# Optimization experiments

Measured on AMD Instinct MI355X. Metric: run time of the kernel, lower is better.

Reference implementation:

```python
import jax, jax.numpy as jnp
import numpy as np

N = 16384      # tokens (batch*seq)
D = 2048       # input_size / d_model
E = 64         # num_experts
K = 2          # top_k
EPS = 1e-12    # F.normalize eps


def setup_inputs() -> dict:
    key = jax.random.key(0)
    k1, k2 = jax.random.split(key)
    x = jax.random.normal(k1, (N, D), dtype=jnp.float32)
    # nn.Linear(input_size, num_experts, bias=False) weight has shape [E, D]
    W = jax.random.normal(k2, (E, D), dtype=jnp.float32) / np.sqrt(D)
    return {"x": x, "W": W}


def reference(x, W):
    # router logits: [N, E], computed (and kept) in float32 as in .float()
    logits = jnp.matmul(x, W.T).astype(jnp.float32)

    top_k_logits, top_k_indices = jax.lax.top_k(logits, K)      # [N, K]
    top_k_gates = jax.nn.softmax(top_k_logits, axis=1).astype(x.dtype)

    # ---- training-mode aux loss ----
    probs = jax.nn.softmax(logits, axis=1)                      # [N, E]
    rows = jnp.arange(logits.shape[0])[:, None]                 # [N, 1]
    gates = jnp.zeros_like(probs).astype(top_k_gates.dtype)
    gates = gates.at[rows, top_k_indices].set(top_k_gates)      # dense [N, E]

    count = logits.shape[0]
    p_sum = probs.sum(axis=0)                                   # [E]
    freq = (gates > 0).astype(jnp.float32).sum(axis=0)          # [E]
    lse = jax.nn.logsumexp(logits, axis=-1)                     # [N]
    lsesq = jnp.sum(lse ** 2)

    p_norm = p_sum / jnp.maximum(jnp.sum(jnp.abs(p_sum)), EPS)   # L1 normalize
    f_norm = freq / jnp.maximum(jnp.sum(jnp.abs(freq)), EPS)
    switchloss = E * jnp.sum(p_norm * f_norm)
    z_loss = lsesq / count
    loss = switchloss + 0.1 * z_loss

    return top_k_indices, top_k_gates, loss
```

## Files before the change

### kernel.cpp

```cpp
#include <hip/hip_runtime.h>
#include <hip/hip_bf16.h>
#include <math.h>

#define N_TOK 16384
#define D_DIM 2048
#define E_EXP 64
#define KQ    256
#define NKS   16
#define NBLK  256

typedef __attribute__((ext_vector_type(8))) short bf16x8;
typedef __attribute__((ext_vector_type(16))) float f32x16;
typedef __attribute__((ext_vector_type(4))) unsigned int u32x4;

#define PACK2(HI, LO) __builtin_amdgcn_perm((HI), (LO), 0x07060302u)

typedef union { unsigned u[4]; bf16x8 v; } b8u;

__global__ void pack_w(const float* __restrict__ W,
                       unsigned short* __restrict__ Wp) {
  const int T = blockIdx.x * 256 + threadIdx.x;
  const int e = T & 63, j = (T >> 6) & 3, c = T >> 8;
  const float* src = W + (size_t)e * D_DIM + c * 32 + j * 8;
  float4 v0 = *(const float4*)src;
  float4 v1 = *(const float4*)(src + 4);
  float vv[8] = {v0.x, v0.y, v0.z, v0.w, v1.x, v1.y, v1.z, v1.w};
  unsigned hu[8], mu[8], lu[8];
#pragma unroll
  for (int q = 0; q < 8; ++q) {
    unsigned u = __float_as_uint(vv[q]);
    unsigned a = u & 0xffff0000u;
    float r = vv[q] - __uint_as_float(a);
    unsigned b = __float_as_uint(r) & 0xffff0000u;
    float r2 = r - __uint_as_float(b);
    unsigned d = __float_as_uint(r2) & 0xffff0000u;
    hu[q] = a; mu[q] = b; lu[q] = d;
  }
  u32x4 ph, pm, pl;
#pragma unroll
  for (int q = 0; q < 4; ++q) {
    ph[q] = PACK2(hu[2 * q + 1], hu[2 * q]);
    pm[q] = PACK2(mu[2 * q + 1], mu[2 * q]);
    pl[q] = PACK2(lu[2 * q + 1], lu[2 * q]);
  }
  const size_t base = (size_t)c * 6144 + (j >> 1) * 3072 + (j & 1) * 512 + e * 8;
  *(u32x4*)(Wp + base)        = ph;
  *(u32x4*)(Wp + base + 1024) = pm;
  *(u32x4*)(Wp + base + 2048) = pl;
}

struct KSst {
  float4 a0, a1, c0, c1;
  bf16x8 B0h, B0m, B0l, B1h, B1m, B1l;
};

__global__ __launch_bounds__(512)
void fused_router(const float* __restrict__ x,
                  const unsigned short* __restrict__ Wp,
                  float* __restrict__ out,
                  double* __restrict__ blk_ps,
                  double* __restrict__ blk_z,
                  unsigned* __restrict__ freq) {
  __shared__ float s_c[2][64][66];
  __shared__ float s_m[64], s_inv[64];
  __shared__ unsigned hist[64];
  const int tid  = threadIdx.x;
  const int lane = tid & 63;
  const int kq   = tid >> 6;
  const int T0   = blockIdx.x * 64;
  if (tid < 64) hist[tid] = 0u;

  const int r  = lane & 31;
  const int kg = lane >> 5;
  const float* xa = x + (size_t)(T0 + r) * D_DIM + kq * KQ + kg * 8;
  const float* xc = xa + (size_t)32 * D_DIM;
  const unsigned short* bq = Wp + (size_t)(kq * 8) * 6144 + kg * 512 + r * 8;

  f32x16 acc00 = (f32x16)0.f, acc01 = (f32x16)0.f;
  f32x16 acc10 = (f32x16)0.f, acc11 = (f32x16)0.f;

#define CVT8(V0, V1, OH, OM, OL)                                            \
  do {                                                                      \
    float vv[8] = {(V0).x, (V0).y, (V0).z, (V0).w,                          \
                   (V1).x, (V1).y, (V1).z, (V1).w};                         \
    unsigned hu[8], mu[8], lu[8];                                           \
    _Pragma("unroll") for (int q = 0; q < 8; ++q) {                         \
      unsigned u = __float_as_uint(vv[q]);                                  \
      unsigned a = u & 0xffff0000u;                                         \
      float rr = vv[q] - __uint_as_float(a);                                \
      unsigned b = __float_as_uint(rr) & 0xffff0000u;                       \
      float r2 = rr - __uint_as_float(b);                                   \
      unsigned d = __float_as_uint(r2) & 0xffff0000u;                       \
      hu[q] = a; mu[q] = b; lu[q] = d;                                      \
    }                                                                       \
    b8u th, tm, tl;                                                         \
    _Pragma("unroll") for (int q = 0; q < 4; ++q) {                         \
      th.u[q] = PACK2(hu[2 * q + 1], hu[2 * q]);                            \
      tm.u[q] = PACK2(mu[2 * q + 1], mu[2 * q]);                            \
      tl.u[q] = PACK2(lu[2 * q + 1], lu[2 * q]);                            \
    }                                                                       \
    OH = th.v; OM = tm.v; OL = tl.v;                                        \
  } while (0)

#define MM6(AH, AM, AL, BH, BM, BL, ACC)                                      \
    ACC = __builtin_amdgcn_mfma_f32_32x32x16_bf16(AH, BH, ACC, 0, 0, 0);      \
    ACC = __builtin_amdgcn_mfma_f32_32x32x16_bf16(AH, BM, ACC, 0, 0, 0);      \
    ACC = __builtin_amdgcn_mfma_f32_32x32x16_bf16(AM, BH, ACC, 0, 0, 0);      \
    ACC = __builtin_amdgcn_mfma_f32_32x32x16_bf16(AH, BL, ACC, 0, 0, 0);      \
    ACC = __builtin_amdgcn_mfma_f32_32x32x16_bf16(AM, BM, ACC, 0, 0, 0);      \
    ACC = __builtin_amdgcn_mfma_f32_32x32x16_bf16(AL, BH, ACC, 0, 0, 0)

#define LOADS(S, KS)                                                        \
  do {                                                                      \
    const float* xp_ = xa + (KS) * 16;                                      \
    const float* xq_ = xc + (KS) * 16;                                      \
    S.a0 = *(const float4*)(xp_);  S.a1 = *(const float4*)(xp_ + 4);        \
    S.c0 = *(const float4*)(xq_);  S.c1 = *(const float4*)(xq_ + 4);        \
    const unsigned short* bk_ = bq + (size_t)(KS) * 3072;                   \
    S.B0h = *(const bf16x8*)(bk_);                                          \
    S.B0m = *(const bf16x8*)(bk_ + 1024);                                   \
    S.B0l = *(const bf16x8*)(bk_ + 2048);                                   \
    S.B1h = *(const bf16x8*)(bk_ + 256);                                    \
    S.B1m = *(const bf16x8*)(bk_ + 256 + 1024);                             \
    S.B1l = *(const bf16x8*)(bk_ + 256 + 2048);                             \
  } while (0)

#define CONSUME(S)                                                          \
  {                                                                         \
    bf16x8 Ah, Am, Al;                                                      \
    CVT8(S.a0, S.a1, Ah, Am, Al);                                           \
    MM6(Ah, Am, Al, S.B0h, S.B0m, S.B0l, acc00);                            \
    MM6(Ah, Am, Al, S.B1h, S.B1m, S.B1l, acc01);                            \
  }                                                                         \
  {                                                                         \
    bf16x8 Ch, Cm, Cl;                                                      \
    CVT8(S.c0, S.c1, Ch, Cm, Cl);                                           \
    MM6(Ch, Cm, Cl, S.B0h, S.B0m, S.B0l, acc10);                            \
    MM6(Ch, Cm, Cl, S.B1h, S.B1m, S.B1l, acc11);                            \
  }

  KSst S0, S1;
  LOADS(S0, 0);
  LOADS(S1, 1);
#pragma unroll
  for (int ks = 0; ks < NKS; ks += 2) {
    CONSUME(S0);
    if (ks + 2 < NKS) LOADS(S0, ks + 2);
    CONSUME(S1);
    if (ks + 3 < NKS) LOADS(S1, ks + 3);
  }
#undef CONSUME
#undef LOADS
#undef MM6
#undef CVT8

  const int slot = kq & 1;
#define SCAT(OP)                                                            \
  _Pragma("unroll") for (int reg = 0; reg < 16; ++reg) {                    \
    const int tl_ = (reg & 3) + 8 * (reg >> 2) + 4 * kg;                    \
    s_c[slot][tl_][r]           OP acc00[reg];                              \
    s_c[slot][tl_][32 + r]      OP acc01[reg];                              \
    s_c[slot][32 + tl_][r]      OP acc10[reg];                              \
    s_c[slot][32 + tl_][32 + r] OP acc11[reg];                              \
  }
  if (kq < 2) SCAT(=);
  __syncthreads();
  if (kq == 2 || kq == 3) SCAT(+=);
  __syncthreads();
  if (kq == 4 || kq == 5) SCAT(+=);
  __syncthreads();
  if (kq == 6 || kq == 7) SCAT(+=);
  __syncthreads();
#undef SCAT
  {
    const int t = tid >> 3, e0 = (tid & 7) * 8;
#pragma unroll
    for (int q = 0; q < 8; ++q)
      s_c[0][t][e0 + q] += s_c[1][t][e0 + q];
  }
  __syncthreads();

  if (tid < 64) {
    const int t = tid;
    float m = -3.402823466e38f;
#pragma unroll
    for (int e = 0; e < 64; ++e) m = fmaxf(m, s_c[0][t][e]);
    float sum = 0.f;
#pragma unroll
    for (int e = 0; e < 64; ++e) sum += __expf(s_c[0][t][e] - m);
    const float lse = m + __logf(sum);
    const float inv = 1.0f / sum;
    s_m[t] = m;
    s_inv[t] = inv;

    float v0 = s_c[0][t][0], v1 = -3.402823466e38f;
    int i0 = 0, i1 = 0;
#pragma unroll
    for (int e = 1; e < 64; ++e) {
      float le = s_c[0][t][e];
      bool g0 = le > v0;
      bool g1 = le > v1;
      float nv1 = g0 ? v0 : (g1 ? le : v1);
      int   ni1 = g0 ? i0 : (g1 ? e  : i1);
      v0 = g0 ? le : v0;
      i0 = g0 ? e  : i0;
      v1 = nv1; i1 = ni1;
    }
    float dd = __expf(v1 - v0);
    float g0 = 1.0f / (1.0f + dd);
    float g1 = dd * g0;

    const int tg = T0 + t;
    out[tg * 2 + 0] = (float)i0;
    out[tg * 2 + 1] = (float)i1;
    out[2 * N_TOK + tg * 2 + 0] = g0;
    out[2 * N_TOK + tg * 2 + 1] = g1;

    atomicAdd(&hist[i0], 1u);
    atomicAdd(&hist[i1], 1u);

    float z = lse * lse;
    z += __shfl_xor(z, 32, 64);
    z += __shfl_xor(z, 16, 64);
    z += __shfl_xor(z, 8, 64);
    z += __shfl_xor(z, 4, 64);
    z += __shfl_xor(z, 2, 64);
    z += __shfl_xor(z, 1, 64);
    if (tid == 0) blk_z[blockIdx.x] = (double)z;
  }
  __syncthreads();

  if (tid >= 64 && tid < 128) {
    const int e = tid - 64;
    float cs2 = 0.f;
#pragma unroll 8
    for (int t = 0; t < 64; ++t)
      cs2 += __expf(s_c[0][t][e] - s_m[t]) * s_inv[t];
    blk_ps[(size_t)blockIdx.x * 64 + e] = (double)cs2;
  }
  if (tid < 64 && hist[tid]) atomicAdd(&freq[tid], hist[tid]);
}

__global__ void finalize(const double* __restrict__ blk_ps,
                         const double* __restrict__ blk_z,
                         const unsigned* __restrict__ freq,
                         float* __restrict__ out_loss) {
  const int lane = threadIdx.x;
  double p = 0.0;
  for (int b = 0; b < NBLK; ++b) p += blk_ps[(size_t)b * 64 + lane];
  double zt = 0.0;
#pragma unroll
  for (int b = 0; b < NBLK / 64; ++b) zt += blk_z[lane * (NBLK / 64) + b];
#pragma unroll
  for (int off = 32; off >= 1; off >>= 1) zt += __shfl_xor(zt, off, 64);

  double f = (double)freq[lane];
  double pa = fabs(p);
  double fa = fabs(f);
#pragma unroll
  for (int off = 32; off >= 1; off >>= 1) {
    pa += __shfl_xor(pa, off, 64);
    fa += __shfl_xor(fa, off, 64);
  }
  pa = pa > 1e-12 ? pa : 1e-12;
  fa = fa > 1e-12 ? fa : 1e-12;

  double s = (p / pa) * (f / fa);
#pragma unroll
  for (int off = 32; off >= 1; off >>= 1) s += __shfl_xor(s, off, 64);

  if (lane == 0) {
    double switchloss = 64.0 * s;
    double z_loss = zt / (double)N_TOK;
    out_loss[0] = (float)(switchloss + 0.1 * z_loss);
  }
}

extern "C" void kernel_launch(void* const* d_in, const int* in_sizes, int n_in,
                              void* d_out, int out_size, void* d_ws, size_t ws_size,
                              hipStream_t stream) {
  const float* x = (const float*)d_in[0];
  const float* W = (const float*)d_in[1];
  float* out = (float*)d_out;

  double* blk_ps = (double*)d_ws;
  double* blk_z  = blk_ps + NBLK * 64;
  unsigned* freq = (unsigned*)(blk_z + NBLK);
  size_t woff = (NBLK * 64 * 8 + NBLK * 8 + 64 * 4 + 255) & ~(size_t)255;
  unsigned short* Wp = (unsigned short*)((char*)d_ws + woff);

  hipMemsetAsync(freq, 0, 64 * sizeof(unsigned), stream);

  pack_w<<<64, 256, 0, stream>>>(W, Wp);
  fused_router<<<NBLK, 512, 0, stream>>>(x, Wp, out, blk_ps, blk_z, freq);
  finalize<<<1, 64, 0, stream>>>(blk_ps, blk_z, freq, out + 4 * N_TOK);
}
```

Before: 59.26 us.

## Split expert halves across wave pairs using 1024-thread blocks

Doubles the block to 16 waves: each K-quarter is now handled by two waves, one per 32-expert half, so each wave keeps two accumulators instead of four and loads only one set of split-bf16 W fragments per step. The goal is lower register pressure and more waves in flight to hide global-load latency. The cost is that every x tile is loaded and converted to three bf16 parts twice, once per expert half, which doubles that conversion work. The float-to-bf16 split is also rewritten in pairwise form, and the final shared-memory reduction is redistributed over 1024 threads.

```diff
diff --git a/kernel.cpp b/kernel.cpp
--- a/kernel.cpp
+++ b/kernel.cpp
@@ -5,7 +5,6 @@
 #define N_TOK 16384
 #define D_DIM 2048
 #define E_EXP 64
-#define KQ    256
 #define NKS   16
 #define NBLK  256
 
@@ -49,12 +48,7 @@
   *(u32x4*)(Wp + base + 2048) = pl;
 }
 
-struct KSst {
-  float4 a0, a1, c0, c1;
-  bf16x8 B0h, B0m, B0l, B1h, B1m, B1l;
-};
-
-__global__ __launch_bounds__(512)
+__global__ __launch_bounds__(1024)
 void fused_router(const float* __restrict__ x,
                   const unsigned short* __restrict__ Wp,
                   float* __restrict__ out,
@@ -66,40 +60,45 @@
   __shared__ unsigned hist[64];
   const int tid  = threadIdx.x;
   const int lane = tid & 63;
-  const int kq   = tid >> 6;
+  const int w    = tid >> 6;
+  const int eh   = w & 1;
+  const int kq   = w >> 1;
   const int T0   = blockIdx.x * 64;
   if (tid < 64) hist[tid] = 0u;
 
   const int r  = lane & 31;
   const int kg = lane >> 5;
-  const float* xa = x + (size_t)(T0 + r) * D_DIM + kq * KQ + kg * 8;
+  const float* xa = x + (size_t)(T0 + r) * D_DIM + kq * 256 + kg * 8;
   const float* xc = xa + (size_t)32 * D_DIM;
-  const unsigned short* bq = Wp + (size_t)(kq * 8) * 6144 + kg * 512 + r * 8;
-
-  f32x16 acc00 = (f32x16)0.f, acc01 = (f32x16)0.f;
-  f32x16 acc10 = (f32x16)0.f, acc11 = (f32x16)0.f;
+  const unsigned short* bq =
+      Wp + (size_t)(kq * 16) * 3072 + kg * 512 + (eh * 32 + r) * 8;
+
+  f32x16 acc0 = (f32x16)0.f;
+  f32x16 acc1 = (f32x16)0.f;
+
+#define CVTP(F0, F1, OH, OM, OL)                                            \
+  do {                                                                      \
+    unsigned a0 = __float_as_uint(F0) & 0xffff0000u;                        \
+    unsigned a1 = __float_as_uint(F1) & 0xffff0000u;                        \
+    float r0 = (F0) - __uint_as_float(a0);                                  \
+    float r1 = (F1) - __uint_as_float(a1);                                  \
+    unsigned b0 = __float_as_uint(r0) & 0xffff0000u;                        \
+    unsigned b1 = __float_as_uint(r1) & 0xffff0000u;                        \
+    float s0 = r0 - __uint_as_float(b0);                                    \
+    float s1 = r1 - __uint_as_float(b1);                                    \
+    unsigned d0 = __float_as_uint(s0) & 0xffff0000u;                        \
+    unsigned d1 = __float_as_uint(s1) & 0xffff0000u;                        \
+    OH = PACK2(a1, a0); OM = PACK2(b1, b0); OL = PACK2(d1, d0);             \
+  } while (0)
 
 #define CVT8(V0, V1, OH, OM, OL)                                            \
   do {                                                                      \
-    float vv[8] = {(V0).x, (V0).y, (V0).z, (V0).w,                          \
-                   (V1).x, (V1).y, (V1).z, (V1).w};                         \
-    unsigned hu[8], mu[8], lu[8];                                           \
-    _Pragma("unroll") for (int q = 0; q < 8; ++q) {                         \
-      unsigned u = __float_as_uint(vv[q]);                                  \
-      unsigned a = u & 0xffff0000u;                                         \
-      float rr = vv[q] - __uint_as_float(a);                                \
-      unsigned b = __float_as_uint(rr) & 0xffff0000u;                       \
-      float r2 = rr - __uint_as_float(b);                                   \
-      unsigned d = __float_as_uint(r2) & 0xffff0000u;                       \
-      hu[q] = a; mu[q] = b; lu[q] = d;                                      \
-    }                                                                       \
-    b8u th, tm, tl;                                                         \
-    _Pragma("unroll") for (int q = 0; q < 4; ++q) {                         \
-      th.u[q] = PACK2(hu[2 * q + 1], hu[2 * q]);                            \
-      tm.u[q] = PACK2(mu[2 * q + 1], mu[2 * q]);                            \
-      tl.u[q] = PACK2(lu[2 * q + 1], lu[2 * q]);                            \
-    }                                                                       \
-    OH = th.v; OM = tm.v; OL = tl.v;                                        \
+    b8u th_, tm_, tl_;                                                      \
+    CVTP((V0).x, (V0).y, th_.u[0], tm_.u[0], tl_.u[0]);                     \
+    CVTP((V0).z, (V0).w, th_.u[1], tm_.u[1], tl_.u[1]);                     \
+    CVTP((V1).x, (V1).y, th_.u[2], tm_.u[2], tl_.u[2]);                     \
+    CVTP((V1).z, (V1).w, th_.u[3], tm_.u[3], tl_.u[3]);                     \
+    OH = th_.v; OM = tm_.v; OL = tl_.v;                                     \
   } while (0)
 
 #define MM6(AH, AM, AL, BH, BM, BL, ACC)                                      \
@@ -110,58 +109,51 @@
     ACC = __builtin_amdgcn_mfma_f32_32x32x16_bf16(AM, BM, ACC, 0, 0, 0);      \
     ACC = __builtin_amdgcn_mfma_f32_32x32x16_bf16(AL, BH, ACC, 0, 0, 0)
 
-#define LOADS(S, KS)                                                        \
+#define LOADX(A0, A1, C0, C1, KS)                                           \
   do {                                                                      \
-    const float* xp_ = xa + (KS) * 16;                                      \
-    const float* xq_ = xc + (KS) * 16;                                      \
-    S.a0 = *(const float4*)(xp_);  S.a1 = *(const float4*)(xp_ + 4);        \
-    S.c0 = *(const float4*)(xq_);  S.c1 = *(const float4*)(xq_ + 4);        \
-    const unsigned short* bk_ = bq + (size_t)(KS) * 3072;                   \
-    S.B0h = *(const bf16x8*)(bk_);                                          \
-    S.B0m = *(const bf16x8*)(bk_ + 1024);                                   \
-    S.B0l = *(const bf16x8*)(bk_ + 2048);                                   \
-    S.B1h = *(const bf16x8*)(bk_ + 256);                                    \
-    S.B1m = *(const bf16x8*)(bk_ + 256 + 1024);                             \
-    S.B1l = *(const bf16x8*)(bk_ + 256 + 2048);                             \
+    A0 = *(const float4*)(xa + (KS) * 16);                                  \
+    A1 = *(const float4*)(xa + (KS) * 16 + 4);                              \
+    C0 = *(const float4*)(xc + (KS) * 16);                                  \
+    C1 = *(const float4*)(xc + (KS) * 16 + 4);                              \
   } while (0)
 
-#define CONSUME(S)                                                          \
+#define CONSUME(A0, A1, C0, C1, KS)                                         \
   {                                                                         \
+    const unsigned short* bk = bq + (size_t)(KS) * 3072;                    \
+    bf16x8 Bh = *(const bf16x8*)(bk);                                       \
+    bf16x8 Bm = *(const bf16x8*)(bk + 1024);                                \
+    bf16x8 Bl = *(const bf16x8*)(bk + 2048);                                \
     bf16x8 Ah, Am, Al;                                                      \
-    CVT8(S.a0, S.a1, Ah, Am, Al);                                           \
-    MM6(Ah, Am, Al, S.B0h, S.B0m, S.B0l, acc00);                            \
-    MM6(Ah, Am, Al, S.B1h, S.B1m, S.B1l, acc01);                            \
-  }                                                                         \
-  {                                                                         \
+    CVT8(A0, A1, Ah, Am, Al);                                               \
+    MM6(Ah, Am, Al, Bh, Bm, Bl, acc0);                                      \
     bf16x8 Ch, Cm, Cl;                                                      \
-    CVT8(S.c0, S.c1, Ch, Cm, Cl);                                           \
-    MM6(Ch, Cm, Cl, S.B0h, S.B0m, S.B0l, acc10);                            \
-    MM6(Ch, Cm, Cl, S.B1h, S.B1m, S.B1l, acc11);                            \
-  }
-
-  KSst S0, S1;
-  LOADS(S0, 0);
-  LOADS(S1, 1);
+    CVT8(C0, C1, Ch, Cm, Cl);                                               \
+    MM6(Ch, Cm, Cl, Bh, Bm, Bl, acc1);                                      \
+  }
+
+  float4 pa0, pa1, pc0, pc1, qa0, qa1, qc0, qc1;
+  LOADX(pa0, pa1, pc0, pc1, 0);
+  LOADX(qa0, qa1, qc0, qc1, 1);
 #pragma unroll
   for (int ks = 0; ks < NKS; ks += 2) {
-    CONSUME(S0);
-    if (ks + 2 < NKS) LOADS(S0, ks + 2);
-    CONSUME(S1);
-    if (ks + 3 < NKS) LOADS(S1, ks + 3);
+    CONSUME(pa0, pa1, pc0, pc1, ks);
+    if (ks + 2 < NKS) LOADX(pa0, pa1, pc0, pc1, ks + 2);
+    CONSUME(qa0, qa1, qc0, qc1, ks + 1);
+    if (ks + 3 < NKS) LOADX(qa0, qa1, qc0, qc1, ks + 3);
   }
 #undef CONSUME
-#undef LOADS
+#undef LOADX
 #undef MM6
 #undef CVT8
+#undef CVTP
 
   const int slot = kq & 1;
+  const int col  = eh * 32 + r;
 #define SCAT(OP)                                                            \
   _Pragma("unroll") for (int reg = 0; reg < 16; ++reg) {                    \
     const int tl_ = (reg & 3) + 8 * (reg >> 2) + 4 * kg;                    \
-    s_c[slot][tl_][r]           OP acc00[reg];                              \
-    s_c[slot][tl_][32 + r]      OP acc01[reg];                              \
-    s_c[slot][32 + tl_][r]      OP acc10[reg];                              \
-    s_c[slot][32 + tl_][32 + r] OP acc11[reg];                              \
+    s_c[slot][tl_][col]      OP acc0[reg];                                  \
+    s_c[slot][32 + tl_][col] OP acc1[reg];                                  \
   }
   if (kq < 2) SCAT(=);
   __syncthreads();
@@ -173,9 +165,9 @@
   __syncthreads();
 #undef SCAT
   {
-    const int t = tid >> 3, e0 = (tid & 7) * 8;
-#pragma unroll
-    for (int q = 0; q < 8; ++q)
+    const int t = tid >> 4, e0 = (tid & 15) * 4;
+#pragma unroll
+    for (int q = 0; q < 4; ++q)
       s_c[0][t][e0 + q] += s_c[1][t][e0 + q];
   }
   __syncthreads();
@@ -292,6 +284,6 @@
   hipMemsetAsync(freq, 0, 64 * sizeof(unsigned), stream);
 
   pack_w<<<64, 256, 0, stream>>>(W, Wp);
-  fused_router<<<NBLK, 512, 0, stream>>>(x, Wp, out, blk_ps, blk_z, freq);
+  fused_router<<<NBLK, 1024, 0, stream>>>(x, Wp, out, blk_ps, blk_z, freq);
   finalize<<<1, 64, 0, stream>>>(blk_ps, blk_z, freq, out + 4 * N_TOK);
 }
```

Measured after the change: 70.27 us. 1.19x slower.
